# Kernel tuning notes

Measured on AMD Instinct MI355X. Metric: run time of the kernel, lower is better.

Reference implementation:

```python
import jax, jax.numpy as jnp
import numpy as np


def setup_inputs() -> dict:
    key = jax.random.key(0)
    k1, k2, k3 = jax.random.split(key, 3)
    B, S, D_in, D_out, R = 4, 4096, 4096, 4096, 16
    x = jax.random.normal(k1, (B, S, D_in), dtype=jnp.float32)
    lora_A = jax.random.normal(k2, (R, D_in), dtype=jnp.float32)
    lora_B = jax.random.normal(k3, (D_out, R), dtype=jnp.float32)
    return {"x": x, "lora_A": lora_A, "lora_B": lora_B}


def reference(x, lora_A, lora_B):
    # Faithful to original: materialize W = lora_B @ lora_A (out, in),
    # then F.linear(x, W) == x @ W.T
    W = lora_B @ lora_A  # [out, in]
    return jnp.einsum("bsi,oi->bso", x, W)
```

## Files before the change

kernel.cpp:

```cpp
#include <hip/hip_runtime.h>


typedef float f4 __attribute__((ext_vector_type(4)));

#define M_TOTAL 16384
#define K_DIM 4096
#define N_DIM 4096
#define R_DIM 16

__device__ float t_buf[M_TOTAL * R_DIM];


#define KC 512

__global__ __launch_bounds__(256, 2)
void lora_phase1(const float* __restrict__ x, const float* __restrict__ A)
{
    __shared__ float A_lds[R_DIM][KC];

    const int tid  = threadIdx.x;
    const int wave = tid >> 6;
    const int lane = tid & 63;
    const int wave_row0 = blockIdx.x * 16 + wave * 4;

    float acc[4][R_DIM];
    #pragma unroll
    for (int w = 0; w < 4; ++w)
        #pragma unroll
        for (int r = 0; r < R_DIM; ++r) acc[w][r] = 0.0f;

    const f4* xr0 = reinterpret_cast<const f4*>(x + (size_t)(wave_row0 + 0) * K_DIM);
    const f4* xr1 = reinterpret_cast<const f4*>(x + (size_t)(wave_row0 + 1) * K_DIM);
    const f4* xr2 = reinterpret_cast<const f4*>(x + (size_t)(wave_row0 + 2) * K_DIM);
    const f4* xr3 = reinterpret_cast<const f4*>(x + (size_t)(wave_row0 + 3) * K_DIM);

    #pragma unroll 1
    for (int c = 0; c < K_DIM / KC; ++c) {
        __syncthreads();
        #pragma unroll
        for (int i = 0; i < 8; ++i) {
            const int r    = wave * 4 + (i >> 1);
            const int half = i & 1;
            f4 v = *reinterpret_cast<const f4*>(
                       A + (size_t)r * K_DIM + c * KC + half * 256 + lane * 4);
            *reinterpret_cast<f4*>(&A_lds[r][half * 256 + lane * 4]) = v;
        }
        __syncthreads();

        #pragma unroll
        for (int s = 0; s < 2; ++s) {
            const int cidx = c * (KC / 4) + s * 64 + lane;
            f4 xv0 = __builtin_nontemporal_load(&xr0[cidx]);
            f4 xv1 = __builtin_nontemporal_load(&xr1[cidx]);
            f4 xv2 = __builtin_nontemporal_load(&xr2[cidx]);
            f4 xv3 = __builtin_nontemporal_load(&xr3[cidx]);
            #pragma unroll
            for (int r = 0; r < R_DIM; ++r) {
                f4 av = *reinterpret_cast<const f4*>(&A_lds[r][s * 256 + lane * 4]);
                acc[0][r] += xv0[0] * av[0] + xv0[1] * av[1] + xv0[2] * av[2] + xv0[3] * av[3];
                acc[1][r] += xv1[0] * av[0] + xv1[1] * av[1] + xv1[2] * av[2] + xv1[3] * av[3];
                acc[2][r] += xv2[0] * av[0] + xv2[1] * av[1] + xv2[2] * av[2] + xv2[3] * av[3];
                acc[3][r] += xv3[0] * av[0] + xv3[1] * av[1] + xv3[2] * av[2] + xv3[3] * av[3];
            }
        }
    }

    #pragma unroll
    for (int w = 0; w < 4; ++w) {
        #pragma unroll
        for (int r = 0; r < R_DIM; ++r) {
            float v = acc[w][r];
            v += __shfl_xor(v, 32, 64);
            v += __shfl_xor(v, 16, 64);
            v += __shfl_xor(v,  8, 64);
            v += __shfl_xor(v,  4, 64);
            v += __shfl_xor(v,  2, 64);
            v += __shfl_xor(v,  1, 64);
            acc[w][r] = v;
        }
    }
    if (lane == 0) {
        #pragma unroll
        for (int w = 0; w < 4; ++w) {
            float* tp = t_buf + (size_t)(wave_row0 + w) * R_DIM;
            #pragma unroll
            for (int rc = 0; rc < 4; ++rc) {
                f4 v = { acc[w][rc * 4 + 0], acc[w][rc * 4 + 1],
                         acc[w][rc * 4 + 2], acc[w][rc * 4 + 3] };
                *reinterpret_cast<f4*>(tp + rc * 4) = v;
            }
        }
    }
}


#define P2_ROWS 64

__global__ __launch_bounds__(256, 2)
void lora_phase2(const float* __restrict__ Bm, float* __restrict__ out)
{
    __shared__ float t_lds[P2_ROWS][R_DIM];

    const int tid  = threadIdx.x;
    const int row0 = (blockIdx.x >> 2) * P2_ROWS;
    const int o0   = (blockIdx.x & 3) * 1024 + tid * 4;

    reinterpret_cast<f4*>(&t_lds[0][0])[tid] =
        reinterpret_cast<const f4*>(t_buf + (size_t)row0 * R_DIM)[tid];

    float br[4][R_DIM];
    #pragma unroll
    for (int oo = 0; oo < 4; ++oo) {
        const f4* bp = reinterpret_cast<const f4*>(Bm + (size_t)(o0 + oo) * R_DIM);
        #pragma unroll
        for (int rc = 0; rc < 4; ++rc) {
            f4 b4 = bp[rc];
            br[oo][rc * 4 + 0] = b4[0];
            br[oo][rc * 4 + 1] = b4[1];
            br[oo][rc * 4 + 2] = b4[2];
            br[oo][rc * 4 + 3] = b4[3];
        }
    }
    __syncthreads();

    #pragma unroll 4
    for (int m = 0; m < P2_ROWS; ++m) {
        float tv[R_DIM];
        const f4* tp = reinterpret_cast<const f4*>(&t_lds[m][0]);
        #pragma unroll
        for (int rc = 0; rc < 4; ++rc) {
            f4 t4 = tp[rc];
            tv[rc * 4 + 0] = t4[0];
            tv[rc * 4 + 1] = t4[1];
            tv[rc * 4 + 2] = t4[2];
            tv[rc * 4 + 3] = t4[3];
        }
        f4 oa = {0.0f, 0.0f, 0.0f, 0.0f};
        #pragma unroll
        for (int r = 0; r < R_DIM; ++r) {
            oa[0] += tv[r] * br[0][r];
            oa[1] += tv[r] * br[1][r];
            oa[2] += tv[r] * br[2][r];
            oa[3] += tv[r] * br[3][r];
        }
        *reinterpret_cast<f4*>(out + (size_t)(row0 + m) * N_DIM + o0) = oa;
    }
}

extern "C" void kernel_launch(void* const* d_in, const int* in_sizes, int n_in,
                              void* d_out, int out_size, void* d_ws, size_t ws_size,
                              hipStream_t stream) {
    const float* x  = (const float*)d_in[0];
    const float* A  = (const float*)d_in[1];
    const float* Bm = (const float*)d_in[2];
    float* out = (float*)d_out;

    lora_phase1<<<dim3(M_TOTAL / 16), dim3(256), 0, stream>>>(x, A);
    lora_phase2<<<dim3((M_TOTAL / P2_ROWS) * 4), dim3(256), 0, stream>>>(Bm, out);
}
```

Measured before the change: 480.1 us.

## Double-buffer A chunks in LDS and prefetch next x/A tiles in phase1

Phase1 now splits K into 256-wide chunks and double-buffers the A tile in LDS. The next chunk's x and A are loaded into registers while the current chunk is being computed. This removes the load-then-sync stall at the start of each chunk and leaves one barrier per iteration instead of two. It costs more registers for the prefetched values and runs twice as many loop iterations, each with less work.

After: 461.1 us. 4.0% less time.

```diff
diff --git a/kernel.cpp b/kernel.cpp
--- a/kernel.cpp
+++ b/kernel.cpp
@@ -11,12 +11,13 @@
 __device__ float t_buf[M_TOTAL * R_DIM];
 
 
-#define KC 512
+#define KC 256
+#define NCHUNK (K_DIM / KC)
 
 __global__ __launch_bounds__(256, 2)
 void lora_phase1(const float* __restrict__ x, const float* __restrict__ A)
 {
-    __shared__ float A_lds[R_DIM][KC];
+    __shared__ float A_lds[2][R_DIM][KC];
 
     const int tid  = threadIdx.x;
     const int wave = tid >> 6;
@@ -34,35 +35,53 @@
     const f4* xr2 = reinterpret_cast<const f4*>(x + (size_t)(wave_row0 + 2) * K_DIM);
     const f4* xr3 = reinterpret_cast<const f4*>(x + (size_t)(wave_row0 + 3) * K_DIM);
 
+    f4 sreg[4];
+    #pragma unroll
+    for (int p = 0; p < 4; ++p)
+        sreg[p] = *reinterpret_cast<const f4*>(A + (size_t)(p * 4 + wave) * K_DIM + lane * 4);
+    #pragma unroll
+    for (int p = 0; p < 4; ++p)
+        *reinterpret_cast<f4*>(&A_lds[0][p * 4 + wave][lane * 4]) = sreg[p];
+
+    f4 xv0 = __builtin_nontemporal_load(&xr0[lane]);
+    f4 xv1 = __builtin_nontemporal_load(&xr1[lane]);
+    f4 xv2 = __builtin_nontemporal_load(&xr2[lane]);
+    f4 xv3 = __builtin_nontemporal_load(&xr3[lane]);
+    __syncthreads();
+
     #pragma unroll 1
-    for (int c = 0; c < K_DIM / KC; ++c) {
-        __syncthreads();
+    for (int c = 0; c < NCHUNK; ++c) {
+        const int cur = c & 1;
+        const bool more = (c + 1 < NCHUNK);
+        f4 xn0, xn1, xn2, xn3;
+        if (more) {
+            const int nidx = (c + 1) * 64 + lane;
+            xn0 = __builtin_nontemporal_load(&xr0[nidx]);
+            xn1 = __builtin_nontemporal_load(&xr1[nidx]);
+            xn2 = __builtin_nontemporal_load(&xr2[nidx]);
+            xn3 = __builtin_nontemporal_load(&xr3[nidx]);
+            #pragma unroll
+            for (int p = 0; p < 4; ++p)
+                sreg[p] = *reinterpret_cast<const f4*>(
+                    A + (size_t)(p * 4 + wave) * K_DIM + (c + 1) * KC + lane * 4);
+        }
+
         #pragma unroll
-        for (int i = 0; i < 8; ++i) {
-            const int r    = wave * 4 + (i >> 1);
-            const int half = i & 1;
-            f4 v = *reinterpret_cast<const f4*>(
-                       A + (size_t)r * K_DIM + c * KC + half * 256 + lane * 4);
-            *reinterpret_cast<f4*>(&A_lds[r][half * 256 + lane * 4]) = v;
+        for (int r = 0; r < R_DIM; ++r) {
+            f4 av = *reinterpret_cast<const f4*>(&A_lds[cur][r][lane * 4]);
+            acc[0][r] += xv0[0] * av[0] + xv0[1] * av[1] + xv0[2] * av[2] + xv0[3] * av[3];
+            acc[1][r] += xv1[0] * av[0] + xv1[1] * av[1] + xv1[2] * av[2] + xv1[3] * av[3];
+            acc[2][r] += xv2[0] * av[0] + xv2[1] * av[1] + xv2[2] * av[2] + xv2[3] * av[3];
+            acc[3][r] += xv3[0] * av[0] + xv3[1] * av[1] + xv3[2] * av[2] + xv3[3] * av[3];
+        }
+
+        if (more) {
+            #pragma unroll
+            for (int p = 0; p < 4; ++p)
+                *reinterpret_cast<f4*>(&A_lds[cur ^ 1][p * 4 + wave][lane * 4]) = sreg[p];
+            xv0 = xn0; xv1 = xn1; xv2 = xn2; xv3 = xn3;
         }
         __syncthreads();
-
-        #pragma unroll
-        for (int s = 0; s < 2; ++s) {
-            const int cidx = c * (KC / 4) + s * 64 + lane;
-            f4 xv0 = __builtin_nontemporal_load(&xr0[cidx]);
-            f4 xv1 = __builtin_nontemporal_load(&xr1[cidx]);
-            f4 xv2 = __builtin_nontemporal_load(&xr2[cidx]);
-            f4 xv3 = __builtin_nontemporal_load(&xr3[cidx]);
-            #pragma unroll
-            for (int r = 0; r < R_DIM; ++r) {
-                f4 av = *reinterpret_cast<const f4*>(&A_lds[r][s * 256 + lane * 4]);
-                acc[0][r] += xv0[0] * av[0] + xv0[1] * av[1] + xv0[2] * av[2] + xv0[3] * av[3];
-                acc[1][r] += xv1[0] * av[0] + xv1[1] * av[1] + xv1[2] * av[2] + xv1[3] * av[3];
-                acc[2][r] += xv2[0] * av[0] + xv2[1] * av[1] + xv2[2] * av[2] + xv2[3] * av[3];
-                acc[3][r] += xv3[0] * av[0] + xv3[1] * av[1] + xv3[2] * av[2] + xv3[3] * av[3];
-            }
-        }
     }
 
     #pragma unroll
```
